# Kernel optimization log

Hardware: AMD Instinct MI355X
Metric: run time of the kernel (lower is better)

## Reference

```python
import jax, jax.numpy as jnp
import numpy as np

B, L, D_IN, D_OUT, H = 8, 1024, 1024, 1024, 16
DH = D_OUT // H                      # 64
SCALE = 1.0 / float(np.sqrt(D_OUT // 2))  # 1/sqrt(512), matches buffer 'scale'
LAMBDA_INIT = 0.8 - 0.6 * float(np.exp(-0.3 * (1 - 1)))  # layer=1 -> 0.2


def _rmsnorm(x, w):
    eps = jnp.finfo(x.dtype).eps
    return x * jax.lax.rsqrt(jnp.mean(x * x, axis=-1, keepdims=True) + eps) * w


def _orth(key, shape):
    a = jax.random.normal(key, shape, dtype=jnp.float32)
    q, r = jnp.linalg.qr(a)
    return q * jnp.sign(jnp.diagonal(r))


def setup_inputs() -> dict:
    key = jax.random.key(0)
    ks = jax.random.split(key, 12)
    return {
        "x": jax.random.normal(ks[0], (B, L, D_IN), dtype=jnp.float32),
        "Wq": _orth(ks[1], (D_OUT, D_IN)), "bq": jnp.zeros((D_OUT,), jnp.float32),
        "Wk": _orth(ks[2], (D_OUT, D_IN)), "bk": jnp.zeros((D_OUT,), jnp.float32),
        "Wv": _orth(ks[3], (D_OUT, D_IN)), "bv": jnp.zeros((D_OUT,), jnp.float32),
        "lambda_params": jnp.full((4,), 0.8, jnp.float32),
        "g1": jnp.ones((D_IN,), jnp.float32),
        "g2": jnp.ones((DH,), jnp.float32),
        "g3": jnp.ones((D_OUT,), jnp.float32),
        "Wf1": _orth(ks[4], (D_OUT, D_OUT)), "bf1": jnp.zeros((D_OUT,), jnp.float32),
        "Wf2": _orth(ks[5], (D_OUT, D_OUT)), "bf2": jnp.zeros((D_OUT,), jnp.float32),
    }


def reference(x, Wq, bq, Wk, bk, Wv, bv, lambda_params, g1, g2, g3, Wf1, bf1, Wf2, bf2):
    xn = _rmsnorm(x, g1)                                   # [B,L,D_in]
    Q = (xn @ Wq.T + bq).reshape(B, L, H, DH)
    K = (xn @ Wk.T + bk).reshape(B, L, H, DH)
    V = (xn @ Wv.T + bv).reshape(B, L, H, DH)
    Q1, Q2 = jnp.split(Q, 2, axis=-1)                      # [B,L,H,DH/2]
    K1, K2 = jnp.split(K, 2, axis=-1)
    phi = jax.nn.elu
    # faithful to source: matmuls on last two dims of [B,L,H,*] -> contract heads per position
    kv1 = SCALE * jnp.einsum('blhd,blhe->blde', phi(K1), V)  # [B,L,DH/2,DH]
    kv2 = SCALE * jnp.einsum('blhd,blhe->blde', phi(K2), V)
    a1 = jnp.einsum('blhd,blde->blhe', phi(Q1), kv1)         # [B,L,H,DH]
    a2 = jnp.einsum('blhd,blde->blhe', phi(Q2), kv2)
    e0 = jnp.exp(lambda_params[0] * lambda_params[1])
    e1 = jnp.exp(lambda_params[2] * lambda_params[3])
    lmbda = e0 - e1 + LAMBDA_INIT
    attn = a1 - lmbda * a2                                  # inverse=False
    attn = (1.0 - LAMBDA_INIT) * _rmsnorm(attn, g2)
    attn = attn.reshape(B, L, D_OUT)
    attn = _rmsnorm(attn, g3) + attn
    h = jax.nn.gelu(attn @ Wf1.T + bf1, approximate=False)  # dropout=0 (eval)
    out = (h @ Wf2.T + bf2) + attn
    return out
```

## Files before the change

### kernel.cpp

```cpp
#include <hip/hip_runtime.h>
#include <cmath>

typedef __bf16 bf16_t;
typedef __attribute__((ext_vector_type(8))) __bf16 bf16x8;
typedef __attribute__((ext_vector_type(4))) __bf16 bf16x4;
typedef __attribute__((ext_vector_type(4))) float f32x4;

#define RMS_EPS 1.1920929e-07f
#define KV_SCALE 0.04419417382415922f

__device__ __forceinline__ void gload16(const void* g, void* l) {
  __builtin_amdgcn_global_load_lds((const __attribute__((address_space(1))) void*)g,
                                   (__attribute__((address_space(3))) void*)l, 16, 0, 0);
}

__global__ __launch_bounds__(256) void cast_all(const float* __restrict__ s0,
                                                const float* __restrict__ s1,
                                                const float* __restrict__ s2,
                                                const float* __restrict__ s3,
                                                const float* __restrict__ s4,
                                                bf16_t* __restrict__ d) {
  const float* srcs[5] = {s0, s1, s2, s3, s4};
  const int which = blockIdx.y;
  const float* src = srcs[which];
  bf16_t* dst = d + ((size_t)which << 20);
  int i = (blockIdx.x * 256 + threadIdx.x) * 4;
  float4 v = *(const float4*)(src + i);
  bf16x4 o;
  o[0] = (bf16_t)v.x; o[1] = (bf16_t)v.y; o[2] = (bf16_t)v.z; o[3] = (bf16_t)v.w;
  *(bf16x4*)(dst + i) = o;
}

__global__ void concat_bias(const float* __restrict__ bq, const float* __restrict__ bk,
                            const float* __restrict__ bv, float* __restrict__ dst) {
  int i = blockIdx.x * 256 + threadIdx.x;
  float v;
  if (i < 1024) v = bq[i];
  else if (i < 2048) v = bk[i - 1024];
  else v = bv[i - 2048];
  dst[i] = v;
}

__global__ __launch_bounds__(256) void rmsnorm_x(const float* __restrict__ x,
                                                 const float* __restrict__ g,
                                                 bf16_t* __restrict__ xn) {
  const int m = blockIdx.x, t = threadIdx.x;
  const float4 v = ((const float4*)(x + (size_t)m * 1024))[t];
  float ss = v.x * v.x + v.y * v.y + v.z * v.z + v.w * v.w;
  #pragma unroll
  for (int o = 1; o < 64; o <<= 1) ss += __shfl_xor(ss, o);
  __shared__ float red[4];
  if ((t & 63) == 0) red[t >> 6] = ss;
  __syncthreads();
  const float r = rsqrtf((red[0] + red[1] + red[2] + red[3]) * (1.f / 1024.f) + RMS_EPS);
  const float4 gv = ((const float4*)g)[t];
  bf16x4 o;
  o[0] = (bf16_t)(v.x * r * gv.x); o[1] = (bf16_t)(v.y * r * gv.y);
  o[2] = (bf16_t)(v.z * r * gv.z); o[3] = (bf16_t)(v.w * r * gv.w);
  *(bf16x4*)(xn + (size_t)m * 1024 + t * 4) = o;
}

template <int MODE>
__global__ __launch_bounds__(512, 2) void gemm2(const bf16_t* __restrict__ A,
                                                const bf16_t* __restrict__ Bm,
                                                const float* __restrict__ bias,
                                                const bf16_t* __restrict__ residb,
                                                void* __restrict__ outp,
                                                int M, int N, int K) {
  __shared__ bf16_t As[4][128][32];
  __shared__ bf16_t Bs[4][256][32];
  const int t = threadIdx.x;
  const int lane = t & 63;
  const int w = t >> 6;
  const int wm = w >> 2;
  const int wn = w & 3;
  const int nTN = N >> 8;

  const int nwg = gridDim.x;
  const int cpx = nwg >> 3;
  int bid = blockIdx.x;
  bid = (bid & 7) * cpx + (bid >> 3);
  const int tm = bid / nTN, tn = bid % nTN;

  const size_t sK = (size_t)K;
  const int NT = K >> 5;

  const int sr = w * 16 + (lane >> 2);
  const int ssw = (((lane & 3) ^ ((lane >> 2) & 3)) << 3);
  const bf16_t* gA  = A  + ((size_t)tm * 128 + sr) * sK + ssw;
  const bf16_t* gB0 = Bm + ((size_t)tn * 256 + sr) * sK + ssw;
  const bf16_t* gB1 = gB0 + (size_t)128 * sK;

  bf16_t* const AsF = &As[0][0][0];
  bf16_t* const BsF = &Bs[0][0][0];
  bf16_t* const dA  = &As[0][w * 16][0];
  bf16_t* const dB0 = &Bs[0][w * 16][0];
  bf16_t* const dB1 = &Bs[0][128 + w * 16][0];

  const int r16 = lane & 15, g4 = lane >> 4;
  const int scol = ((g4 ^ (r16 & 3)) << 3);
  const int loA = (wm * 64 + r16) * 32 + scol;
  const int loB = (wn * 64 + r16) * 32 + scol;

  f32x4 acc[4][4];
  #pragma unroll
  for (int i = 0; i < 4; ++i)
    #pragma unroll
    for (int j = 0; j < 4; ++j) acc[i][j] = (f32x4){0.f, 0.f, 0.f, 0.f};

  auto STAGE = [&](int tt) {
    const int sl = tt & 3;
    const size_t ko = (size_t)tt << 5;
    gload16(gA  + ko, dA  + sl * 4096);
    gload16(gB0 + ko, dB0 + sl * 8192);
    gload16(gB1 + ko, dB1 + sl * 8192);
  };
  auto READ = [&](int tt, bf16x8* aa, bf16x8* bb) {
    const int sl = tt & 3;
    const bf16_t* pa = AsF + sl * 4096 + loA;
    const bf16_t* pb = BsF + sl * 8192 + loB;
    aa[0] = *(const bf16x8*)(pa);        aa[1] = *(const bf16x8*)(pa + 512);
    aa[2] = *(const bf16x8*)(pa + 1024); aa[3] = *(const bf16x8*)(pa + 1536);
    bb[0] = *(const bf16x8*)(pb);        bb[1] = *(const bf16x8*)(pb + 512);
    bb[2] = *(const bf16x8*)(pb + 1024); bb[3] = *(const bf16x8*)(pb + 1536);
  };
  auto BODY = [&](int tt, bf16x8* ca, bf16x8* cb, bf16x8* na, bf16x8* nb) {
    if (tt + 4 <= NT) {
      STAGE(tt + 3);
      asm volatile("s_waitcnt vmcnt(6)" ::: "memory");
    } else if (tt == NT - 3) {
      asm volatile("s_waitcnt vmcnt(3)" ::: "memory");
    } else if (tt == NT - 2) {
      asm volatile("s_waitcnt vmcnt(0)" ::: "memory");
    }
    __syncthreads();
    if (tt + 1 < NT) READ(tt + 1, na, nb);
    __builtin_amdgcn_s_setprio(1);
    #pragma unroll
    for (int mi = 0; mi < 4; ++mi)
      #pragma unroll
      for (int nj = 0; nj < 4; ++nj)
        acc[mi][nj] = __builtin_amdgcn_mfma_f32_16x16x32_bf16(ca[mi], cb[nj], acc[mi][nj], 0, 0, 0);
    __builtin_amdgcn_s_setprio(0);
  };

  bf16x8 fa0[4], fb0[4], fa1[4], fb1[4];
  STAGE(0); STAGE(1); STAGE(2);
  asm volatile("s_waitcnt vmcnt(6)" ::: "memory");
  __syncthreads();
  READ(0, fa0, fb0);
  for (int tt = 0; tt < NT; tt += 2) {
    BODY(tt,     fa0, fb0, fa1, fb1);
    BODY(tt + 1, fa1, fb1, fa0, fb0);
  }

  const int hi4 = g4 * 4;
  #pragma unroll
  for (int mi = 0; mi < 4; ++mi) {
    #pragma unroll
    for (int nj = 0; nj < 4; ++nj) {
      const int gc = tn * 256 + wn * 64 + nj * 16 + r16;
      const float bv = bias[gc];
      #pragma unroll
      for (int r = 0; r < 4; ++r) {
        const int gr = tm * 128 + wm * 64 + mi * 16 + hi4 + r;
        float v = acc[mi][nj][r] + bv;
        if constexpr (MODE == 0) {
          ((bf16_t*)outp)[(size_t)gr * N + gc] = (bf16_t)v;
        } else if constexpr (MODE == 1) {
          v = 0.5f * v * (1.0f + erff(v * 0.70710678118654752f));
          ((bf16_t*)outp)[(size_t)gr * N + gc] = (bf16_t)v;
        } else {
          v += (float)residb[(size_t)gr * N + gc];
          ((float*)outp)[(size_t)gr * N + gc] = v;
        }
      }
    }
  }
}

__global__ __launch_bounds__(256) void attn_fused(const bf16_t* __restrict__ qkv,
                                                  const float* __restrict__ lp,
                                                  const float* __restrict__ g2,
                                                  const float* __restrict__ g3,
                                                  bf16_t* __restrict__ attnb) {
  __shared__ __align__(16) char lds[4][6656];
  const int t = threadIdx.x;
  const int lane = t & 63;
  const int w = t >> 6;
  const int m = blockIdx.x * 4 + w;
  char* const sQ  = lds[w];
  char* const sK  = lds[w] + 2048;
  char* const sVt = lds[w] + 4096;
  char* const sSb = lds[w] + 6144;

  const float lmbda = __expf(lp[0] * lp[1]) - __expf(lp[2] * lp[3]) + 0.2f;
  const int l7 = lane & 7, l8 = lane >> 3;
  const bf16x8* src = (const bf16x8*)(qkv + (size_t)m * 3072);

  const float qsc = (l7 < 4) ? KV_SCALE : -lmbda * KV_SCALE;
  #pragma unroll
  for (int c = 0; c < 2; ++c) {
    bf16x8 v = src[c * 64 + lane];
    const int h = c * 8 + l8;
    bf16x8 o;
    #pragma unroll
    for (int i = 0; i < 8; ++i) {
      float f = (float)v[i];
      f = f > 0.f ? f : __expf(f) - 1.f;
      o[i] = (bf16_t)(f * qsc);
    }
    *(bf16x8*)(sQ + ((h * 128 + 16 * l7) ^ ((h & 7) << 4))) = o;
  }
  #pragma unroll
  for (int c = 2; c < 4; ++c) {
    bf16x8 v = src[c * 64 + lane];
    const int h = (c - 2) * 8 + l8;
    bf16x8 o;
    #pragma unroll
    for (int i = 0; i < 8; ++i) {
      float f = (float)v[i];
      f = f > 0.f ? f : __expf(f) - 1.f;
      o[i] = (bf16_t)f;
    }
    *(bf16x8*)(sK + ((h * 128 + 16 * l7) ^ ((h & 7) << 4))) = o;
  }
  #pragma unroll
  for (int c = 4; c < 6; ++c) {
    bf16x8 v = src[c * 64 + lane];
    const int h = (c - 4) * 8 + l8;
    #pragma unroll
    for (int i = 0; i < 8; ++i) {
      const int e = 8 * l7 + i;
      *(bf16_t*)(sVt + ((e * 32 + h * 2) ^ ((e & 1) << 4))) = v[i];
    }
  }

  const int r16 = lane & 15, g4 = lane >> 4;
  f32x4 accS = {};
  {
    const int ra = r16 * 128;
    const int sw = (r16 & 7) << 4;
    bf16x8 a0 = *(const bf16x8*)(sQ + ((ra + 16 * g4) ^ sw));
    bf16x8 b0 = *(const bf16x8*)(sK + ((ra + 16 * g4) ^ sw));
    bf16x8 a1 = *(const bf16x8*)(sQ + ((ra + 64 + 16 * g4) ^ sw));
    bf16x8 b1 = *(const bf16x8*)(sK + ((ra + 64 + 16 * g4) ^ sw));
    accS = __builtin_amdgcn_mfma_f32_16x16x32_bf16(a0, b0, accS, 0, 0, 0);
    accS = __builtin_amdgcn_mfma_f32_16x16x32_bf16(a1, b1, accS, 0, 0, 0);
  }

  #pragma unroll
  for (int r = 0; r < 4; ++r) {
    const int h = g4 * 4 + r;
    *(bf16_t*)(sSb + ((h * 32 + 2 * r16) ^ ((h & 1) << 4))) = (bf16_t)accS[r];
  }

  bf16x8 zf = {};
  bf16x8 aS = zf;
  if (lane < 32) aS = *(const bf16x8*)(sSb + ((r16 * 32 + 16 * g4) ^ ((r16 & 1) << 4)));
  f32x4 accA[4];
  #pragma unroll
  for (int j = 0; j < 4; ++j) {
    bf16x8 bV = zf;
    if (lane < 32) {
      const int row = j * 16 + r16;
      bV = *(const bf16x8*)(sVt + ((row * 32 + 16 * g4) ^ ((row & 1) << 4)));
    }
    f32x4 z4 = {};
    accA[j] = __builtin_amdgcn_mfma_f32_16x16x32_bf16(aS, bV, z4, 0, 0, 0);
  }

  float rnh[4];
  #pragma unroll
  for (int r = 0; r < 4; ++r) {
    float s = 0.f;
    #pragma unroll
    for (int j = 0; j < 4; ++j) s += accA[j][r] * accA[j][r];
    #pragma unroll
    for (int o = 1; o < 16; o <<= 1) s += __shfl_xor(s, o);
    rnh[r] = rsqrtf(s * (1.f / 64.f) + RMS_EPS);
  }
  float g2v[4];
  #pragma unroll
  for (int j = 0; j < 4; ++j) g2v[j] = g2[j * 16 + r16];
  float val[4][4];
  float tot = 0.f;
  #pragma unroll
  for (int j = 0; j < 4; ++j)
    #pragma unroll
    for (int r = 0; r < 4; ++r) {
      const float vv = accA[j][r] * rnh[r] * g2v[j] * 0.8f;
      val[j][r] = vv;
      tot += vv * vv;
    }
  #pragma unroll
  for (int o = 1; o < 64; o <<= 1) tot += __shfl_xor(tot, o);
  const float rn2 = rsqrtf(tot * (1.f / 1024.f) + RMS_EPS);

  bf16_t* dst = attnb + (size_t)m * 1024;
  #pragma unroll
  for (int j = 0; j < 4; ++j)
    #pragma unroll
    for (int r = 0; r < 4; ++r) {
      const int n = (g4 * 4 + r) * 64 + j * 16 + r16;
      const float ov = val[j][r] * rn2 * g3[n] + val[j][r];
      dst[n] = (bf16_t)ov;
    }
}

extern "C" void kernel_launch(void* const* d_in, const int* in_sizes, int n_in,
                              void* d_out, int out_size, void* d_ws, size_t ws_size,
                              hipStream_t stream) {
  const float* x   = (const float*)d_in[0];
  const float* Wq  = (const float*)d_in[1];
  const float* bq  = (const float*)d_in[2];
  const float* Wk  = (const float*)d_in[3];
  const float* bk  = (const float*)d_in[4];
  const float* Wv  = (const float*)d_in[5];
  const float* bv  = (const float*)d_in[6];
  const float* lp  = (const float*)d_in[7];
  const float* g1  = (const float*)d_in[8];
  const float* g2  = (const float*)d_in[9];
  const float* g3  = (const float*)d_in[10];
  const float* Wf1 = (const float*)d_in[11];
  const float* bf1 = (const float*)d_in[12];
  const float* Wf2 = (const float*)d_in[13];
  const float* bf2 = (const float*)d_in[14];

  char* ws = (char*)d_ws;
  bf16_t* wqkv  = (bf16_t*)(ws + 0);
  bf16_t* wf1b  = (bf16_t*)(ws + 6291456);
  bf16_t* wf2b  = (bf16_t*)(ws + 8388608);
  float*  bqkv  = (float*)(ws + 10485760);
  bf16_t* xn    = (bf16_t*)(ws + 10498048);
  bf16_t* qkv   = (bf16_t*)(ws + 27275264);
  bf16_t* attnb = (bf16_t*)(ws + 77606912);
  bf16_t* hbuf  = (bf16_t*)(ws + 94384128);

  cast_all<<<dim3(1024, 5), 256, 0, stream>>>(Wq, Wk, Wv, Wf1, Wf2, wqkv);
  concat_bias<<<12, 256, 0, stream>>>(bq, bk, bv, bqkv);
  rmsnorm_x<<<8192, 256, 0, stream>>>(x, g1, xn);
  gemm2<0><<<768, 512, 0, stream>>>(xn, wqkv, bqkv, nullptr, (void*)qkv, 8192, 3072, 1024);
  attn_fused<<<2048, 256, 0, stream>>>(qkv, lp, g2, g3, attnb);
  gemm2<1><<<256, 512, 0, stream>>>(attnb, wf1b, bf1, nullptr, (void*)hbuf, 8192, 1024, 1024);
  gemm2<2><<<256, 512, 0, stream>>>(hbuf, wf2b, bf2, attnb, d_out, 8192, 1024, 1024);
}
```

Measured before the change: 289.5 us.

## Switch GEMMs to 128x128 tiles with 256 threads and 3-stage LDS pipeline

Replaces the 128x256 tile, 512-thread GEMM with a 128x128 tile, 4-wave kernel that uses a 3-slot LDS ring (two tiles in flight) instead of 4 slots, and changes the LDS swizzle pattern. It launches twice as many workgroups and targets 3 workgroups per CU, which is meant to improve occupancy and load balance, particularly for the 1024-wide FFN GEMMs that previously had only 256 workgroups. In exchange, each tile reuses its loaded data less and prefetch depth is shallower, which raises global/L2 traffic per flop.

```diff
diff --git a/kernel.cpp b/kernel.cpp
--- a/kernel.cpp
+++ b/kernel.cpp
@@ -61,20 +61,19 @@
 }
 
 template <int MODE>
-__global__ __launch_bounds__(512, 2) void gemm2(const bf16_t* __restrict__ A,
+__global__ __launch_bounds__(256, 3) void gemm3(const bf16_t* __restrict__ A,
                                                 const bf16_t* __restrict__ Bm,
                                                 const float* __restrict__ bias,
                                                 const bf16_t* __restrict__ residb,
                                                 void* __restrict__ outp,
                                                 int M, int N, int K) {
-  __shared__ bf16_t As[4][128][32];
-  __shared__ bf16_t Bs[4][256][32];
+  __shared__ bf16_t As[3][128][32];
+  __shared__ bf16_t Bs[3][128][32];
   const int t = threadIdx.x;
   const int lane = t & 63;
   const int w = t >> 6;
-  const int wm = w >> 2;
-  const int wn = w & 3;
-  const int nTN = N >> 8;
+  const int wm = w >> 1, wn = w & 1;
+  const int nTN = N >> 7;
 
   const int nwg = gridDim.x;
   const int cpx = nwg >> 3;
@@ -85,20 +84,21 @@
   const size_t sK = (size_t)K;
   const int NT = K >> 5;
 
-  const int sr = w * 16 + (lane >> 2);
-  const int ssw = (((lane & 3) ^ ((lane >> 2) & 3)) << 3);
+  const int sr = t >> 2;
+  const int ssw = (((t & 3) ^ ((t >> 3) & 3)) << 3);
   const bf16_t* gA  = A  + ((size_t)tm * 128 + sr) * sK + ssw;
-  const bf16_t* gB0 = Bm + ((size_t)tn * 256 + sr) * sK + ssw;
-  const bf16_t* gB1 = gB0 + (size_t)128 * sK;
-
+  const bf16_t* gA1 = gA + (size_t)64 * sK;
+  const bf16_t* gB  = Bm + ((size_t)tn * 128 + sr) * sK + ssw;
+  const bf16_t* gB1 = gB + (size_t)64 * sK;
+  bf16_t* const dA0 = &As[0][w * 16][0];
+  bf16_t* const dA1 = &As[0][64 + w * 16][0];
+  bf16_t* const dB0 = &Bs[0][w * 16][0];
+  bf16_t* const dB1 = &Bs[0][64 + w * 16][0];
   bf16_t* const AsF = &As[0][0][0];
   bf16_t* const BsF = &Bs[0][0][0];
-  bf16_t* const dA  = &As[0][w * 16][0];
-  bf16_t* const dB0 = &Bs[0][w * 16][0];
-  bf16_t* const dB1 = &Bs[0][128 + w * 16][0];
 
   const int r16 = lane & 15, g4 = lane >> 4;
-  const int scol = ((g4 ^ (r16 & 3)) << 3);
+  const int scol = ((g4 ^ ((r16 >> 1) & 3)) << 3);
   const int loA = (wm * 64 + r16) * 32 + scol;
   const int loB = (wn * 64 + r16) * 32 + scol;
 
@@ -108,33 +108,40 @@
     #pragma unroll
     for (int j = 0; j < 4; ++j) acc[i][j] = (f32x4){0.f, 0.f, 0.f, 0.f};
 
-  auto STAGE = [&](int tt) {
-    const int sl = tt & 3;
+  auto STAGE = [&](int tt, int sl) {
     const size_t ko = (size_t)tt << 5;
-    gload16(gA  + ko, dA  + sl * 4096);
-    gload16(gB0 + ko, dB0 + sl * 8192);
-    gload16(gB1 + ko, dB1 + sl * 8192);
+    const int so = sl * 4096;
+    gload16(gA  + ko, dA0 + so);
+    gload16(gA1 + ko, dA1 + so);
+    gload16(gB  + ko, dB0 + so);
+    gload16(gB1 + ko, dB1 + so);
   };
-  auto READ = [&](int tt, bf16x8* aa, bf16x8* bb) {
-    const int sl = tt & 3;
+  auto READ = [&](int sl, bf16x8* aa, bf16x8* bb) {
     const bf16_t* pa = AsF + sl * 4096 + loA;
-    const bf16_t* pb = BsF + sl * 8192 + loB;
+    const bf16_t* pb = BsF + sl * 4096 + loB;
     aa[0] = *(const bf16x8*)(pa);        aa[1] = *(const bf16x8*)(pa + 512);
     aa[2] = *(const bf16x8*)(pa + 1024); aa[3] = *(const bf16x8*)(pa + 1536);
     bb[0] = *(const bf16x8*)(pb);        bb[1] = *(const bf16x8*)(pb + 512);
     bb[2] = *(const bf16x8*)(pb + 1024); bb[3] = *(const bf16x8*)(pb + 1536);
   };
+
+  int sl_w = 2;
+  int sl_r = 1;
   auto BODY = [&](int tt, bf16x8* ca, bf16x8* cb, bf16x8* na, bf16x8* nb) {
-    if (tt + 4 <= NT) {
-      STAGE(tt + 3);
-      asm volatile("s_waitcnt vmcnt(6)" ::: "memory");
-    } else if (tt == NT - 3) {
-      asm volatile("s_waitcnt vmcnt(3)" ::: "memory");
-    } else if (tt == NT - 2) {
+    if (tt + 2 < NT) {
+      STAGE(tt + 2, sl_w);
+      sl_w = (sl_w == 2) ? 0 : sl_w + 1;
+      asm volatile("s_waitcnt vmcnt(4)" ::: "memory");
+    } else if (tt + 2 == NT) {
       asm volatile("s_waitcnt vmcnt(0)" ::: "memory");
     }
-    __syncthreads();
-    if (tt + 1 < NT) READ(tt + 1, na, nb);
+    asm volatile("" ::: "memory");
+    __builtin_amdgcn_s_barrier();
+    asm volatile("" ::: "memory");
+    if (tt + 1 < NT) {
+      READ(sl_r, na, nb);
+      sl_r = (sl_r == 2) ? 0 : sl_r + 1;
+    }
     __builtin_amdgcn_s_setprio(1);
     #pragma unroll
     for (int mi = 0; mi < 4; ++mi)
@@ -145,9 +152,11 @@
   };
 
   bf16x8 fa0[4], fb0[4], fa1[4], fb1[4];
-  STAGE(0); STAGE(1); STAGE(2);
-  asm volatile("s_waitcnt vmcnt(6)" ::: "memory");
-  __syncthreads();
+  STAGE(0, 0); STAGE(1, 1);
+  asm volatile("s_waitcnt vmcnt(4)" ::: "memory");
+  asm volatile("" ::: "memory");
+  __builtin_amdgcn_s_barrier();
+  asm volatile("" ::: "memory");
   READ(0, fa0, fb0);
   for (int tt = 0; tt < NT; tt += 2) {
     BODY(tt,     fa0, fb0, fa1, fb1);
@@ -159,7 +168,7 @@
   for (int mi = 0; mi < 4; ++mi) {
     #pragma unroll
     for (int nj = 0; nj < 4; ++nj) {
-      const int gc = tn * 256 + wn * 64 + nj * 16 + r16;
+      const int gc = tn * 128 + wn * 64 + nj * 16 + r16;
       const float bv = bias[gc];
       #pragma unroll
       for (int r = 0; r < 4; ++r) {
@@ -340,8 +349,8 @@
   cast_all<<<dim3(1024, 5), 256, 0, stream>>>(Wq, Wk, Wv, Wf1, Wf2, wqkv);
   concat_bias<<<12, 256, 0, stream>>>(bq, bk, bv, bqkv);
   rmsnorm_x<<<8192, 256, 0, stream>>>(x, g1, xn);
-  gemm2<0><<<768, 512, 0, stream>>>(xn, wqkv, bqkv, nullptr, (void*)qkv, 8192, 3072, 1024);
+  gemm3<0><<<1536, 256, 0, stream>>>(xn, wqkv, bqkv, nullptr, (void*)qkv, 8192, 3072, 1024);
   attn_fused<<<2048, 256, 0, stream>>>(qkv, lp, g2, g3, attnb);
-  gemm2<1><<<256, 512, 0, stream>>>(attnb, wf1b, bf1, nullptr, (void*)hbuf, 8192, 1024, 1024);
-  gemm2<2><<<256, 512, 0, stream>>>(hbuf, wf2b, bf2, attnb, d_out, 8192, 1024, 1024);
-}
+  gemm3<1><<<512, 256, 0, stream>>>(attnb, wf1b, bf1, nullptr, (void*)hbuf, 8192, 1024, 1024);
+  gemm3<2><<<512, 256, 0, stream>>>(hbuf, wf2b, bf2, attnb, d_out, 8192, 1024, 1024);
+}
```

After: 260.6 us. 1.11x faster.

## Restructure GEMM main loop into 8-phase interleaved load/MFMA schedule with BK=64

Applied to the files above, without the earlier changes.

Rewrites the bf16 GEMM mainloop to use a K-tile of 64 with a 3-slot LDS ring instead of 32 with 4 slots. Each K-tile is split into four phases that interleave LDS fragment reads, partial global->LDS staging, and 8-MFMA groups separated by explicit barriers. The goal is finer overlap of global loads, LDS reads and matrix ops, plus halving the number of outer iterations. In exchange it adds many more barriers per tile, and LDS use grows to 144KB per block, which may limit the launch_bounds target of 2 blocks per CU.

```diff
diff --git a/kernel.cpp b/kernel.cpp
--- a/kernel.cpp
+++ b/kernel.cpp
@@ -60,20 +60,40 @@
   *(bf16x4*)(xn + (size_t)m * 1024 + t * 4) = o;
 }
 
+#define BAR  do { asm volatile("" ::: "memory"); __builtin_amdgcn_s_barrier(); \
+                  asm volatile("" ::: "memory"); } while (0)
+#define LGKM0 asm volatile("s_waitcnt lgkmcnt(0)" ::: "memory")
+#define MFMA8(B0, B1, NJ0, NJ1) do { \
+  __builtin_amdgcn_s_setprio(1); \
+  acc[0][NJ0] = __builtin_amdgcn_mfma_f32_16x16x32_bf16(a0, B0, acc[0][NJ0], 0, 0, 0); \
+  acc[1][NJ0] = __builtin_amdgcn_mfma_f32_16x16x32_bf16(a1, B0, acc[1][NJ0], 0, 0, 0); \
+  acc[2][NJ0] = __builtin_amdgcn_mfma_f32_16x16x32_bf16(a2, B0, acc[2][NJ0], 0, 0, 0); \
+  acc[3][NJ0] = __builtin_amdgcn_mfma_f32_16x16x32_bf16(a3, B0, acc[3][NJ0], 0, 0, 0); \
+  acc[0][NJ1] = __builtin_amdgcn_mfma_f32_16x16x32_bf16(a0, B1, acc[0][NJ1], 0, 0, 0); \
+  acc[1][NJ1] = __builtin_amdgcn_mfma_f32_16x16x32_bf16(a1, B1, acc[1][NJ1], 0, 0, 0); \
+  acc[2][NJ1] = __builtin_amdgcn_mfma_f32_16x16x32_bf16(a2, B1, acc[2][NJ1], 0, 0, 0); \
+  acc[3][NJ1] = __builtin_amdgcn_mfma_f32_16x16x32_bf16(a3, B1, acc[3][NJ1], 0, 0, 0); \
+  __builtin_amdgcn_s_setprio(0); } while (0)
+#define STA(TT, SL)   do { const size_t ko = (size_t)(TT) << 6; \
+  gload16(gA0 + ko, dA0 + (SL) * 8192);  gload16(gA1 + ko, dA1 + (SL) * 8192); } while (0)
+#define STB01(TT, SL) do { const size_t ko = (size_t)(TT) << 6; \
+  gload16(gB0 + ko, dB0 + (SL) * 16384); gload16(gB1 + ko, dB1 + (SL) * 16384); } while (0)
+#define STB23(TT, SL) do { const size_t ko = (size_t)(TT) << 6; \
+  gload16(gB2 + ko, dB2 + (SL) * 16384); gload16(gB3 + ko, dB3 + (SL) * 16384); } while (0)
+
 template <int MODE>
-__global__ __launch_bounds__(512, 2) void gemm2(const bf16_t* __restrict__ A,
-                                                const bf16_t* __restrict__ Bm,
-                                                const float* __restrict__ bias,
-                                                const bf16_t* __restrict__ residb,
-                                                void* __restrict__ outp,
-                                                int M, int N, int K) {
-  __shared__ bf16_t As[4][128][32];
-  __shared__ bf16_t Bs[4][256][32];
+__global__ __launch_bounds__(512, 2) void gemm8p(const bf16_t* __restrict__ A,
+                                                 const bf16_t* __restrict__ Bm,
+                                                 const float* __restrict__ bias,
+                                                 const bf16_t* __restrict__ residb,
+                                                 void* __restrict__ outp,
+                                                 int M, int N, int K) {
+  __shared__ bf16_t sA[3][128][64];
+  __shared__ bf16_t sB[3][256][64];
   const int t = threadIdx.x;
   const int lane = t & 63;
   const int w = t >> 6;
-  const int wm = w >> 2;
-  const int wn = w & 3;
+  const int wm = w >> 2, wn = w & 3;
   const int nTN = N >> 8;
 
   const int nwg = gridDim.x;
@@ -83,24 +103,29 @@
   const int tm = bid / nTN, tn = bid % nTN;
 
   const size_t sK = (size_t)K;
-  const int NT = K >> 5;
-
-  const int sr = w * 16 + (lane >> 2);
-  const int ssw = (((lane & 3) ^ ((lane >> 2) & 3)) << 3);
-  const bf16_t* gA  = A  + ((size_t)tm * 128 + sr) * sK + ssw;
-  const bf16_t* gB0 = Bm + ((size_t)tn * 256 + sr) * sK + ssw;
-  const bf16_t* gB1 = gB0 + (size_t)128 * sK;
-
-  bf16_t* const AsF = &As[0][0][0];
-  bf16_t* const BsF = &Bs[0][0][0];
-  bf16_t* const dA  = &As[0][w * 16][0];
-  bf16_t* const dB0 = &Bs[0][w * 16][0];
-  bf16_t* const dB1 = &Bs[0][128 + w * 16][0];
+  const int NT = K >> 6;
+
+  const int srow = t >> 3;
+  const int selem = (((t & 7) ^ (srow & 7)) << 3);
+  const bf16_t* gA0 = A  + ((size_t)tm * 128 + srow) * sK + selem;
+  const bf16_t* gA1 = gA0 + (size_t)64 * sK;
+  const bf16_t* gB0 = Bm + ((size_t)tn * 256 + srow) * sK + selem;
+  const bf16_t* gB1 = gB0 + (size_t)64 * sK;
+  const bf16_t* gB2 = gB0 + (size_t)128 * sK;
+  const bf16_t* gB3 = gB0 + (size_t)192 * sK;
+  bf16_t* const dA0 = &sA[0][w * 8][0];
+  bf16_t* const dA1 = &sA[0][64 + w * 8][0];
+  bf16_t* const dB0 = &sB[0][w * 8][0];
+  bf16_t* const dB1 = &sB[0][64 + w * 8][0];
+  bf16_t* const dB2 = &sB[0][128 + w * 8][0];
+  bf16_t* const dB3 = &sB[0][192 + w * 8][0];
 
   const int r16 = lane & 15, g4 = lane >> 4;
-  const int scol = ((g4 ^ (r16 & 3)) << 3);
-  const int loA = (wm * 64 + r16) * 32 + scol;
-  const int loB = (wn * 64 + r16) * 32 + scol;
+  const int e7 = r16 & 7;
+  const int ck0 = ((g4 ^ e7) << 3);
+  const int ck1 = (((4 | g4) ^ e7) << 3);
+  const bf16_t* const rA = &sA[0][wm * 64 + r16][0];
+  const bf16_t* const rB = &sB[0][wn * 64 + r16][0];
 
   f32x4 acc[4][4];
   #pragma unroll
@@ -108,50 +133,52 @@
     #pragma unroll
     for (int j = 0; j < 4; ++j) acc[i][j] = (f32x4){0.f, 0.f, 0.f, 0.f};
 
-  auto STAGE = [&](int tt) {
-    const int sl = tt & 3;
-    const size_t ko = (size_t)tt << 5;
-    gload16(gA  + ko, dA  + sl * 4096);
-    gload16(gB0 + ko, dB0 + sl * 8192);
-    gload16(gB1 + ko, dB1 + sl * 8192);
-  };
-  auto READ = [&](int tt, bf16x8* aa, bf16x8* bb) {
-    const int sl = tt & 3;
-    const bf16_t* pa = AsF + sl * 4096 + loA;
-    const bf16_t* pb = BsF + sl * 8192 + loB;
-    aa[0] = *(const bf16x8*)(pa);        aa[1] = *(const bf16x8*)(pa + 512);
-    aa[2] = *(const bf16x8*)(pa + 1024); aa[3] = *(const bf16x8*)(pa + 1536);
-    bb[0] = *(const bf16x8*)(pb);        bb[1] = *(const bf16x8*)(pb + 512);
-    bb[2] = *(const bf16x8*)(pb + 1024); bb[3] = *(const bf16x8*)(pb + 1536);
-  };
-  auto BODY = [&](int tt, bf16x8* ca, bf16x8* cb, bf16x8* na, bf16x8* nb) {
-    if (tt + 4 <= NT) {
-      STAGE(tt + 3);
-      asm volatile("s_waitcnt vmcnt(6)" ::: "memory");
-    } else if (tt == NT - 3) {
-      asm volatile("s_waitcnt vmcnt(3)" ::: "memory");
-    } else if (tt == NT - 2) {
-      asm volatile("s_waitcnt vmcnt(0)" ::: "memory");
-    }
-    __syncthreads();
-    if (tt + 1 < NT) READ(tt + 1, na, nb);
-    __builtin_amdgcn_s_setprio(1);
-    #pragma unroll
-    for (int mi = 0; mi < 4; ++mi)
-      #pragma unroll
-      for (int nj = 0; nj < 4; ++nj)
-        acc[mi][nj] = __builtin_amdgcn_mfma_f32_16x16x32_bf16(ca[mi], cb[nj], acc[mi][nj], 0, 0, 0);
-    __builtin_amdgcn_s_setprio(0);
-  };
-
-  bf16x8 fa0[4], fb0[4], fa1[4], fb1[4];
-  STAGE(0); STAGE(1); STAGE(2);
+  STA(0, 0); STB01(0, 0); STB23(0, 0);
+  STA(1, 1); STB01(1, 1); STB23(1, 1);
   asm volatile("s_waitcnt vmcnt(6)" ::: "memory");
-  __syncthreads();
-  READ(0, fa0, fb0);
-  for (int tt = 0; tt < NT; tt += 2) {
-    BODY(tt,     fa0, fb0, fa1, fb1);
-    BODY(tt + 1, fa1, fb1, fa0, fb0);
+  BAR;
+
+  bf16x8 a0, a1, a2, a3, b0, b1;
+  int slc = 0;
+  for (int tt = 0; tt < NT; ++tt) {
+    const int sls = (slc >= 1) ? slc - 1 : 2;
+    const bool st = (tt + 2 < NT);
+    const bf16_t* pa = rA + slc * 8192;
+    const bf16_t* pb = rB + slc * 16384;
+    a0 = *(const bf16x8*)(pa + ck0);
+    a1 = *(const bf16x8*)(pa + 1024 + ck0);
+    a2 = *(const bf16x8*)(pa + 2048 + ck0);
+    a3 = *(const bf16x8*)(pa + 3072 + ck0);
+    b0 = *(const bf16x8*)(pb + ck0);
+    b1 = *(const bf16x8*)(pb + 1024 + ck0);
+    if (st) STA(tt + 2, sls);
+    BAR; LGKM0;
+    MFMA8(b0, b1, 0, 1);
+    BAR;
+    b0 = *(const bf16x8*)(pb + 2048 + ck0);
+    b1 = *(const bf16x8*)(pb + 3072 + ck0);
+    if (st) STB01(tt + 2, sls);
+    BAR; LGKM0;
+    MFMA8(b0, b1, 2, 3);
+    BAR;
+    a0 = *(const bf16x8*)(pa + ck1);
+    a1 = *(const bf16x8*)(pa + 1024 + ck1);
+    a2 = *(const bf16x8*)(pa + 2048 + ck1);
+    a3 = *(const bf16x8*)(pa + 3072 + ck1);
+    b0 = *(const bf16x8*)(pb + ck1);
+    b1 = *(const bf16x8*)(pb + 1024 + ck1);
+    if (st) STB23(tt + 2, sls);
+    BAR; LGKM0;
+    MFMA8(b0, b1, 0, 1);
+    BAR;
+    b0 = *(const bf16x8*)(pb + 2048 + ck1);
+    b1 = *(const bf16x8*)(pb + 3072 + ck1);
+    if (st) { asm volatile("s_waitcnt vmcnt(6)" ::: "memory"); }
+    else if (tt + 2 == NT) { asm volatile("s_waitcnt vmcnt(0)" ::: "memory"); }
+    BAR; LGKM0;
+    MFMA8(b0, b1, 2, 3);
+    BAR;
+    slc = (slc + 1 >= 3) ? 0 : slc + 1;
   }
 
   const int hi4 = g4 * 4;
@@ -340,8 +367,8 @@
   cast_all<<<dim3(1024, 5), 256, 0, stream>>>(Wq, Wk, Wv, Wf1, Wf2, wqkv);
   concat_bias<<<12, 256, 0, stream>>>(bq, bk, bv, bqkv);
   rmsnorm_x<<<8192, 256, 0, stream>>>(x, g1, xn);
-  gemm2<0><<<768, 512, 0, stream>>>(xn, wqkv, bqkv, nullptr, (void*)qkv, 8192, 3072, 1024);
+  gemm8p<0><<<768, 512, 0, stream>>>(xn, wqkv, bqkv, nullptr, (void*)qkv, 8192, 3072, 1024);
   attn_fused<<<2048, 256, 0, stream>>>(qkv, lp, g2, g3, attnb);
-  gemm2<1><<<256, 512, 0, stream>>>(attnb, wf1b, bf1, nullptr, (void*)hbuf, 8192, 1024, 1024);
-  gemm2<2><<<256, 512, 0, stream>>>(hbuf, wf2b, bf2, attnb, d_out, 8192, 1024, 1024);
-}
+  gemm8p<1><<<256, 512, 0, stream>>>(attnb, wf1b, bf1, nullptr, (void*)hbuf, 8192, 1024, 1024);
+  gemm8p<2><<<256, 512, 0, stream>>>(hbuf, wf2b, bf2, attnb, d_out, 8192, 1024, 1024);
+}
```

Result: faster. 279.5 us (-3.4%).
